# Optimization experiments

Hardware: AMD Instinct MI355X
Metric: run time of the kernel (lower is better)

## Reference

```python
import jax, jax.numpy as jnp
import numpy as np

BATCH, IN_F, OUT_F = 8192, 2048, 2048
LN2 = float(np.log(2.0))


def setup_inputs() -> dict:
    key = jax.random.key(0)
    kx, kw = jax.random.split(key)
    x = jax.random.normal(kx, (BATCH, IN_F), dtype=jnp.float32)
    # kaiming_uniform_(a=sqrt(5)) on (OUT_F, IN_F+1): U(-1/sqrt(fan_in), 1/sqrt(fan_in))
    bound = 1.0 / np.sqrt(IN_F + 1)
    W = jax.random.uniform(kw, (OUT_F, IN_F + 1), dtype=jnp.float32,
                           minval=-bound, maxval=bound)
    W = W.at[:, -1].set(0.0)  # bias column initialized to 0
    return {"x": x, "W": W}


def reference(x, W):
    # UniversalKANNode forward, node_type='add', use_bias=True,
    # function = lshifted_softplus: f(x, w) = w * (softplus(x) - ln2)
    # Append bias ones column: (B, IN_F+1)
    xb = jnp.concatenate([x, jnp.ones((x.shape[0], 1), dtype=x.dtype)], axis=-1)
    phi = jax.nn.softplus(xb) - jnp.asarray(LN2, dtype=x.dtype)  # (B, IN_F+1)
    # sum over input dim of W[o,i] * phi[b,i]  ==  GEMM
    return jnp.einsum("bi,oi->bo", phi, W)  # (B, OUT_F)
```

## Files before the change

### kernel.cpp

```cpp
#include <hip/hip_runtime.h>

#define M_DIM 8192
#define N_DIM 2048
#define K_DIM 2048
#define LN2F 0.69314718055994530942f
#define LOG2EF 1.44269504088896340736f
#define BIAS_PHI 0.62009741f

typedef _Float16 f16x8 __attribute__((ext_vector_type(8)));
typedef float f32x4 __attribute__((ext_vector_type(4)));

__device__ __forceinline__ float softplus_m_ln2(float v) {
    float t = v * LOG2EF;
    float e = __builtin_amdgcn_exp2f(t);
    float r = (__builtin_amdgcn_logf(1.0f + e) - 1.0f) * LN2F;
    return t < 24.0f ? r : v - LN2F;
}

__global__ __launch_bounds__(256) void prep_kernel(const float* __restrict__ x,
                                                   const float* __restrict__ W,
                                                   _Float16* __restrict__ phi,
                                                   _Float16* __restrict__ Wh,
                                                   float* __restrict__ bias) {
    if (blockIdx.x < 8192) {
        size_t i = ((size_t)blockIdx.x * blockDim.x + threadIdx.x) * 8;
        float4 v0 = *(const float4*)(x + i);
        float4 v1 = *(const float4*)(x + i + 4);
        union { _Float16 h[8]; uint4 u; } pk;
        pk.h[0] = (_Float16)softplus_m_ln2(v0.x);
        pk.h[1] = (_Float16)softplus_m_ln2(v0.y);
        pk.h[2] = (_Float16)softplus_m_ln2(v0.z);
        pk.h[3] = (_Float16)softplus_m_ln2(v0.w);
        pk.h[4] = (_Float16)softplus_m_ln2(v1.x);
        pk.h[5] = (_Float16)softplus_m_ln2(v1.y);
        pk.h[6] = (_Float16)softplus_m_ln2(v1.z);
        pk.h[7] = (_Float16)softplus_m_ln2(v1.w);
        *(uint4*)(phi + i) = pk.u;
    } else {
        const int o = blockIdx.x - 8192;
        const float* row = W + (size_t)o * (K_DIM + 1) + threadIdx.x * 8;
        union { _Float16 h[8]; uint4 u; } pk;
#pragma unroll
        for (int j = 0; j < 8; ++j)
            pk.h[j] = (_Float16)row[j];
        *(uint4*)(Wh + (size_t)o * K_DIM + threadIdx.x * 8) = pk.u;
        if (threadIdx.x == 0)
            bias[o] = W[(size_t)o * (K_DIM + 1) + K_DIM] * BIAS_PHI;
    }
}

__global__ __launch_bounds__(256, 2) void kan_gemm(const _Float16* __restrict__ A,
                                                   const _Float16* __restrict__ B,
                                                   const float* __restrict__ bias,
                                                   float* __restrict__ C) {
    __shared__ __align__(16) _Float16 sA[256 * 64];
    __shared__ __align__(16) _Float16 sB[128 * 64];

    const int tid  = threadIdx.x;
    const int lane = tid & 63;
    const int wv   = tid >> 6;

    const size_t Arow0 = (size_t)blockIdx.x * 256;
    const size_t Brow0 = (size_t)blockIdx.y * 128;

    const int r8 = lane >> 3;
    const int lc = (lane & 7) ^ r8;

    const _Float16* gA = A + (Arow0 + wv * 64 + r8) * (size_t)K_DIM + lc * 8;
    _Float16* sAw = &sA[wv * 64 * 64];
    const _Float16* gB = B + (Brow0 + wv * 32 + r8) * (size_t)K_DIM + lc * 8;
    _Float16* sBw = &sB[wv * 32 * 64];

    const int wr = (wv >> 1) * 128;
    const int wc = (wv & 1) * 64;
    const int lr   = lane & 15;
    const int kph0 = ((lane >> 4) ^ (lr & 7)) * 8;

    f32x4 acc[8][4];
#pragma unroll
    for (int i = 0; i < 8; ++i)
#pragma unroll
        for (int j = 0; j < 4; ++j)
            acc[i][j] = (f32x4){0.0f, 0.0f, 0.0f, 0.0f};

    for (int k0 = 0; k0 < K_DIM; k0 += 64) {
        __syncthreads();
#pragma unroll
        for (int j = 0; j < 8; ++j)
            __builtin_amdgcn_global_load_lds(
                (const __attribute__((address_space(1))) void*)(gA + k0 + (size_t)j * 8 * K_DIM),
                (__attribute__((address_space(3))) void*)(sAw + j * 8 * 64), 16, 0, 0);
#pragma unroll
        for (int j = 0; j < 4; ++j)
            __builtin_amdgcn_global_load_lds(
                (const __attribute__((address_space(1))) void*)(gB + k0 + (size_t)j * 8 * K_DIM),
                (__attribute__((address_space(3))) void*)(sBw + j * 8 * 64), 16, 0, 0);
        __syncthreads();

#pragma unroll
        for (int kc = 0; kc < 2; ++kc) {
            const int ko = kph0 ^ (kc * 32);
            f16x8 bfr[4];
#pragma unroll
            for (int ni = 0; ni < 4; ++ni)
                bfr[ni] = *(const f16x8*)&sB[(wc + ni * 16 + lr) * 64 + ko];

#pragma unroll
            for (int mh = 0; mh < 2; ++mh) {
                f16x8 af[4];
#pragma unroll
                for (int mi = 0; mi < 4; ++mi)
                    af[mi] = *(const f16x8*)&sA[(wr + (mh * 4 + mi) * 16 + lr) * 64 + ko];
#pragma unroll
                for (int mi = 0; mi < 4; ++mi)
#pragma unroll
                    for (int ni = 0; ni < 4; ++ni)
                        acc[mh * 4 + mi][ni] = __builtin_amdgcn_mfma_f32_16x16x32_f16(
                            af[mi], bfr[ni], acc[mh * 4 + mi][ni], 0, 0, 0);
            }
        }
    }

    const int crow = (lane >> 4) * 4;
    float bsv[4];
#pragma unroll
    for (int ni = 0; ni < 4; ++ni)
        bsv[ni] = bias[Brow0 + wc + ni * 16 + lr];

#pragma unroll
    for (int mi = 0; mi < 8; ++mi) {
#pragma unroll
        for (int r = 0; r < 4; ++r) {
            float* cp = C + (Arow0 + wr + mi * 16 + crow + r) * (size_t)N_DIM
                        + Brow0 + wc + lr;
#pragma unroll
            for (int ni = 0; ni < 4; ++ni)
                cp[ni * 16] = acc[mi][ni][r] + bsv[ni];
        }
    }
}

extern "C" void kernel_launch(void* const* d_in, const int* in_sizes, int n_in,
                              void* d_out, int out_size, void* d_ws, size_t ws_size,
                              hipStream_t stream) {
    const float* x = (const float*)d_in[0];
    const float* W = (const float*)d_in[1];
    float* out = (float*)d_out;

    char* ws = (char*)d_ws;
    _Float16* phi = (_Float16*)ws;
    _Float16* Wh  = (_Float16*)(ws + (size_t)M_DIM * K_DIM * sizeof(_Float16));
    float* bias   = (float*)(ws + (size_t)M_DIM * K_DIM * sizeof(_Float16)
                                + (size_t)N_DIM * K_DIM * sizeof(_Float16));

    prep_kernel<<<8192 + 2048, 256, 0, stream>>>(x, W, phi, Wh, bias);
    dim3 grid(M_DIM / 256, N_DIM / 128);
    kan_gemm<<<grid, 256, 0, stream>>>(phi, Wh, bias, out);
}
```

Measured before the change: 185.6 us.

## Double-buffer GEMM LDS tiles with 8-wave 256x256 blocks and interleaved prefetch

The GEMM moves from 4 waves on a 256x128 tile to 8 waves on a 256x256 tile. The LDS A and B tiles are double-buffered, and the next K-slice's global-to-LDS loads are spread across four MFMA phases separated by barriers and raised s_setprio. The aim is to hide global load latency behind MFMA work, which the old single-buffer loop exposed with two barriers per iteration, and to improve data reuse per block. In exchange, LDS use grows to 128KB per block, which likely allows only one block per CU despite launch_bounds(512,2). Each iteration also now has more barriers.

```diff
diff --git a/kernel.cpp b/kernel.cpp
--- a/kernel.cpp
+++ b/kernel.cpp
@@ -49,30 +49,31 @@
     }
 }
 
-__global__ __launch_bounds__(256, 2) void kan_gemm(const _Float16* __restrict__ A,
+#define GLL(gp, lp)                                                                     \
+    __builtin_amdgcn_global_load_lds((const __attribute__((address_space(1))) void*)(gp), \
+                                     (__attribute__((address_space(3))) void*)(lp), 16, 0, 0)
+
+__global__ __launch_bounds__(512, 2) void kan_gemm(const _Float16* __restrict__ A,
                                                    const _Float16* __restrict__ B,
                                                    const float* __restrict__ bias,
                                                    float* __restrict__ C) {
-    __shared__ __align__(16) _Float16 sA[256 * 64];
-    __shared__ __align__(16) _Float16 sB[128 * 64];
+    __shared__ __align__(16) _Float16 sA[2][256 * 64];
+    __shared__ __align__(16) _Float16 sB[2][256 * 64];
 
     const int tid  = threadIdx.x;
     const int lane = tid & 63;
     const int wv   = tid >> 6;
+    const int wm   = wv >> 2;
+    const int wn   = wv & 3;
 
     const size_t Arow0 = (size_t)blockIdx.x * 256;
-    const size_t Brow0 = (size_t)blockIdx.y * 128;
+    const size_t Bcol0 = (size_t)blockIdx.y * 256;
 
     const int r8 = lane >> 3;
     const int lc = (lane & 7) ^ r8;
-
-    const _Float16* gA = A + (Arow0 + wv * 64 + r8) * (size_t)K_DIM + lc * 8;
-    _Float16* sAw = &sA[wv * 64 * 64];
-    const _Float16* gB = B + (Brow0 + wv * 32 + r8) * (size_t)K_DIM + lc * 8;
-    _Float16* sBw = &sB[wv * 32 * 64];
-
-    const int wr = (wv >> 1) * 128;
-    const int wc = (wv & 1) * 64;
+    const _Float16* gA = A + (Arow0 + wv * 32 + r8) * (size_t)K_DIM + lc * 8;
+    const _Float16* gB = B + (Bcol0 + wv * 32 + r8) * (size_t)K_DIM + lc * 8;
+
     const int lr   = lane & 15;
     const int kph0 = ((lane >> 4) ^ (lr & 7)) * 8;
 
@@ -83,56 +84,139 @@
         for (int j = 0; j < 4; ++j)
             acc[i][j] = (f32x4){0.0f, 0.0f, 0.0f, 0.0f};
 
-    for (int k0 = 0; k0 < K_DIM; k0 += 64) {
-        __syncthreads();
-#pragma unroll
-        for (int j = 0; j < 8; ++j)
-            __builtin_amdgcn_global_load_lds(
-                (const __attribute__((address_space(1))) void*)(gA + k0 + (size_t)j * 8 * K_DIM),
-                (__attribute__((address_space(3))) void*)(sAw + j * 8 * 64), 16, 0, 0);
-#pragma unroll
-        for (int j = 0; j < 4; ++j)
-            __builtin_amdgcn_global_load_lds(
-                (const __attribute__((address_space(1))) void*)(gB + k0 + (size_t)j * 8 * K_DIM),
-                (__attribute__((address_space(3))) void*)(sBw + j * 8 * 64), 16, 0, 0);
-        __syncthreads();
-
-#pragma unroll
-        for (int kc = 0; kc < 2; ++kc) {
-            const int ko = kph0 ^ (kc * 32);
-            f16x8 bfr[4];
-#pragma unroll
-            for (int ni = 0; ni < 4; ++ni)
-                bfr[ni] = *(const f16x8*)&sB[(wc + ni * 16 + lr) * 64 + ko];
-
-#pragma unroll
-            for (int mh = 0; mh < 2; ++mh) {
-                f16x8 af[4];
-#pragma unroll
-                for (int mi = 0; mi < 4; ++mi)
-                    af[mi] = *(const f16x8*)&sA[(wr + (mh * 4 + mi) * 16 + lr) * 64 + ko];
-#pragma unroll
-                for (int mi = 0; mi < 4; ++mi)
-#pragma unroll
-                    for (int ni = 0; ni < 4; ++ni)
-                        acc[mh * 4 + mi][ni] = __builtin_amdgcn_mfma_f32_16x16x32_f16(
-                            af[mi], bfr[ni], acc[mh * 4 + mi][ni], 0, 0, 0);
-            }
-        }
+#pragma unroll
+    for (int j = 0; j < 4; ++j)
+        GLL(gA + (size_t)j * 8 * K_DIM, &sA[0][(wv * 32 + j * 8) * 64]);
+#pragma unroll
+    for (int j = 0; j < 4; ++j)
+        GLL(gB + (size_t)j * 8 * K_DIM, &sB[0][(wv * 32 + j * 8) * 64]);
+    asm volatile("s_waitcnt vmcnt(0)" ::: "memory");
+    __builtin_amdgcn_s_barrier();
+
+    f16x8 afr[4][2];
+    f16x8 bfr[2][2];
+
+    for (int t = 0; t < 32; ++t) {
+        const int d = t & 1;
+        const _Float16* sAd = sA[d];
+        const _Float16* sBd = sB[d];
+        _Float16* dA = sA[d ^ 1];
+        _Float16* dB = sB[d ^ 1];
+        const size_t kn = (size_t)(t + 1) * 64;
+        const bool more = (t + 1) < 32;
+
+#pragma unroll
+        for (int mi = 0; mi < 4; ++mi)
+#pragma unroll
+            for (int kc = 0; kc < 2; ++kc)
+                afr[mi][kc] = *(const f16x8*)&sAd[(wm * 128 + mi * 16 + lr) * 64 + (kph0 ^ (kc * 32))];
+#pragma unroll
+        for (int ni = 0; ni < 2; ++ni)
+#pragma unroll
+            for (int kc = 0; kc < 2; ++kc)
+                bfr[ni][kc] = *(const f16x8*)&sBd[(wn * 64 + ni * 16 + lr) * 64 + (kph0 ^ (kc * 32))];
+        if (more) {
+            GLL(gA + kn + (size_t)0 * 8 * K_DIM, &dA[(wv * 32 + 0) * 64]);
+            GLL(gA + kn + (size_t)1 * 8 * K_DIM, &dA[(wv * 32 + 8) * 64]);
+        }
+        __builtin_amdgcn_s_barrier();
+        asm volatile("s_waitcnt lgkmcnt(0)" ::: "memory");
+        __builtin_amdgcn_s_setprio(1);
+#pragma unroll
+        for (int kc = 0; kc < 2; ++kc)
+#pragma unroll
+            for (int mi = 0; mi < 4; ++mi)
+#pragma unroll
+                for (int ni = 0; ni < 2; ++ni)
+                    acc[mi][ni] = __builtin_amdgcn_mfma_f32_16x16x32_f16(
+                        afr[mi][kc], bfr[ni][kc], acc[mi][ni], 0, 0, 0);
+        __builtin_amdgcn_s_setprio(0);
+        __builtin_amdgcn_s_barrier();
+
+#pragma unroll
+        for (int ni = 0; ni < 2; ++ni)
+#pragma unroll
+            for (int kc = 0; kc < 2; ++kc)
+                bfr[ni][kc] = *(const f16x8*)&sBd[(wn * 64 + 32 + ni * 16 + lr) * 64 + (kph0 ^ (kc * 32))];
+        if (more) {
+            GLL(gA + kn + (size_t)2 * 8 * K_DIM, &dA[(wv * 32 + 16) * 64]);
+            GLL(gA + kn + (size_t)3 * 8 * K_DIM, &dA[(wv * 32 + 24) * 64]);
+        }
+        __builtin_amdgcn_s_barrier();
+        asm volatile("s_waitcnt lgkmcnt(0)" ::: "memory");
+        __builtin_amdgcn_s_setprio(1);
+#pragma unroll
+        for (int kc = 0; kc < 2; ++kc)
+#pragma unroll
+            for (int mi = 0; mi < 4; ++mi)
+#pragma unroll
+                for (int ni = 0; ni < 2; ++ni)
+                    acc[mi][2 + ni] = __builtin_amdgcn_mfma_f32_16x16x32_f16(
+                        afr[mi][kc], bfr[ni][kc], acc[mi][2 + ni], 0, 0, 0);
+        __builtin_amdgcn_s_setprio(0);
+        __builtin_amdgcn_s_barrier();
+
+#pragma unroll
+        for (int mi = 0; mi < 4; ++mi)
+#pragma unroll
+            for (int kc = 0; kc < 2; ++kc)
+                afr[mi][kc] = *(const f16x8*)&sAd[(wm * 128 + 64 + mi * 16 + lr) * 64 + (kph0 ^ (kc * 32))];
+        if (more) {
+            GLL(gB + kn + (size_t)0 * 8 * K_DIM, &dB[(wv * 32 + 0) * 64]);
+            GLL(gB + kn + (size_t)1 * 8 * K_DIM, &dB[(wv * 32 + 8) * 64]);
+        }
+        __builtin_amdgcn_s_barrier();
+        asm volatile("s_waitcnt lgkmcnt(0)" ::: "memory");
+        __builtin_amdgcn_s_setprio(1);
+#pragma unroll
+        for (int kc = 0; kc < 2; ++kc)
+#pragma unroll
+            for (int mi = 0; mi < 4; ++mi)
+#pragma unroll
+                for (int ni = 0; ni < 2; ++ni)
+                    acc[4 + mi][2 + ni] = __builtin_amdgcn_mfma_f32_16x16x32_f16(
+                        afr[mi][kc], bfr[ni][kc], acc[4 + mi][2 + ni], 0, 0, 0);
+        __builtin_amdgcn_s_setprio(0);
+        __builtin_amdgcn_s_barrier();
+
+#pragma unroll
+        for (int ni = 0; ni < 2; ++ni)
+#pragma unroll
+            for (int kc = 0; kc < 2; ++kc)
+                bfr[ni][kc] = *(const f16x8*)&sBd[(wn * 64 + ni * 16 + lr) * 64 + (kph0 ^ (kc * 32))];
+        if (more) {
+            GLL(gB + kn + (size_t)2 * 8 * K_DIM, &dB[(wv * 32 + 16) * 64]);
+            GLL(gB + kn + (size_t)3 * 8 * K_DIM, &dB[(wv * 32 + 24) * 64]);
+        }
+        __builtin_amdgcn_s_barrier();
+        asm volatile("s_waitcnt lgkmcnt(0)" ::: "memory");
+        __builtin_amdgcn_s_setprio(1);
+#pragma unroll
+        for (int kc = 0; kc < 2; ++kc)
+#pragma unroll
+            for (int mi = 0; mi < 4; ++mi)
+#pragma unroll
+                for (int ni = 0; ni < 2; ++ni)
+                    acc[4 + mi][ni] = __builtin_amdgcn_mfma_f32_16x16x32_f16(
+                        afr[mi][kc], bfr[ni][kc], acc[4 + mi][ni], 0, 0, 0);
+        __builtin_amdgcn_s_setprio(0);
+
+        asm volatile("s_waitcnt vmcnt(0)" ::: "memory");
+        __builtin_amdgcn_s_barrier();
     }
 
     const int crow = (lane >> 4) * 4;
     float bsv[4];
 #pragma unroll
     for (int ni = 0; ni < 4; ++ni)
-        bsv[ni] = bias[Brow0 + wc + ni * 16 + lr];
+        bsv[ni] = bias[Bcol0 + wn * 64 + ni * 16 + lr];
 
 #pragma unroll
     for (int mi = 0; mi < 8; ++mi) {
 #pragma unroll
         for (int r = 0; r < 4; ++r) {
-            float* cp = C + (Arow0 + wr + mi * 16 + crow + r) * (size_t)N_DIM
-                        + Brow0 + wc + lr;
+            float* cp = C + (Arow0 + wm * 128 + mi * 16 + crow + r) * (size_t)N_DIM
+                        + Bcol0 + wn * 64 + lr;
 #pragma unroll
             for (int ni = 0; ni < 4; ++ni)
                 cp[ni * 16] = acc[mi][ni][r] + bsv[ni];
@@ -154,6 +238,6 @@
                                 + (size_t)N_DIM * K_DIM * sizeof(_Float16));
 
     prep_kernel<<<8192 + 2048, 256, 0, stream>>>(x, W, phi, Wh, bias);
-    dim3 grid(M_DIM / 256, N_DIM / 128);
-    kan_gemm<<<grid, 256, 0, stream>>>(phi, Wh, bias, out);
-}
+    dim3 grid(M_DIM / 256, N_DIM / 256);
+    kan_gemm<<<grid, 512, 0, stream>>>(phi, Wh, bias, out);
+}
```

Result: no change. 188.1 us (+1.3%).

## Rewrite GEMM as 256x256 tile, 8-wave, double-buffered LDS pipeline with interleaved loads

Applied to the files above, without the earlier changes.

The GEMM tile grows from 256x128 to 256x256 with 512 threads (8 waves in a 2x4 layout). LDS is double-buffered, and global-to-LDS loads are interleaved with MFMA quadrants using explicit vmcnt/lgkmcnt waits, barriers and setprio, in a ping-pong style schedule. The aim is to hide global load latency behind MFMA work and to raise arithmetic intensity per tile. In exchange, LDS use grows to 128KB per block and the hand-tuned wait counts are fragile; an error in them would produce wrong results.

```diff
diff --git a/kernel.cpp b/kernel.cpp
--- a/kernel.cpp
+++ b/kernel.cpp
@@ -49,30 +49,80 @@
     }
 }
 
-__global__ __launch_bounds__(256, 2) void kan_gemm(const _Float16* __restrict__ A,
+#define GLL(gp, lp)                                                                     \
+    __builtin_amdgcn_global_load_lds((const __attribute__((address_space(1))) void*)(gp), \
+                                     (__attribute__((address_space(3))) void*)(lp), 16, 0, 0)
+
+#define BAR   __builtin_amdgcn_s_barrier()
+#define LGKM0 asm volatile("s_waitcnt lgkmcnt(0)" ::: "memory")
+#define VM(n) asm volatile("s_waitcnt vmcnt(" #n ")" ::: "memory")
+#define PRIO1 __builtin_amdgcn_s_setprio(1)
+#define PRIO0 __builtin_amdgcn_s_setprio(0)
+
+#define READ_A(dst, d, roff)                                                             \
+    _Pragma("unroll") for (int kc = 0; kc < 2; ++kc)                                     \
+    _Pragma("unroll") for (int mi = 0; mi < 4; ++mi)                                     \
+        dst[mi][kc] = *(const f16x8*)&sA[d][(wm * 128 + (roff) + mi * 16 + lr) * 64 + (kph0 ^ (kc * 32))];
+
+#define READ_B(dst, d, coff)                                                             \
+    _Pragma("unroll") for (int kc = 0; kc < 2; ++kc)                                     \
+    _Pragma("unroll") for (int ni = 0; ni < 2; ++ni)                                     \
+        dst[ni][kc] = *(const f16x8*)&sB[d][(wn * 64 + (coff) + ni * 16 + lr) * 64 + (kph0 ^ (kc * 32))];
+
+#define MFMA_Q(AF, BF, AI, BJ)                                                           \
+    _Pragma("unroll") for (int kc = 0; kc < 2; ++kc)                                     \
+    _Pragma("unroll") for (int mi = 0; mi < 4; ++mi)                                     \
+    _Pragma("unroll") for (int ni = 0; ni < 2; ++ni)                                     \
+        acc[(AI) + mi][(BJ) + ni] = __builtin_amdgcn_mfma_f32_16x16x32_f16(              \
+            AF[mi][kc], BF[ni][kc], acc[(AI) + mi][(BJ) + ni], 0, 0, 0);
+
+#define GLL_A(half, buf, kt)                                                             \
+    do {                                                                                 \
+        GLL(gAj[2 * (half)] + (size_t)(kt) * 64, &sA[buf][rA[2 * (half)] * 64]);         \
+        GLL(gAj[2 * (half) + 1] + (size_t)(kt) * 64, &sA[buf][rA[2 * (half) + 1] * 64]); \
+    } while (0)
+#define GLL_B(half, buf, kt)                                                             \
+    do {                                                                                 \
+        GLL(gBj[2 * (half)] + (size_t)(kt) * 64, &sB[buf][rB[2 * (half)] * 64]);         \
+        GLL(gBj[2 * (half) + 1] + (size_t)(kt) * 64, &sB[buf][rB[2 * (half) + 1] * 64]); \
+    } while (0)
+
+__global__ __launch_bounds__(512, 2) void kan_gemm(const _Float16* __restrict__ A,
                                                    const _Float16* __restrict__ B,
                                                    const float* __restrict__ bias,
                                                    float* __restrict__ C) {
-    __shared__ __align__(16) _Float16 sA[256 * 64];
-    __shared__ __align__(16) _Float16 sB[128 * 64];
+    __shared__ __align__(16) _Float16 sA[2][256 * 64];
+    __shared__ __align__(16) _Float16 sB[2][256 * 64];
 
     const int tid  = threadIdx.x;
     const int lane = tid & 63;
     const int wv   = tid >> 6;
+    const int wm   = wv >> 2;
+    const int wn   = wv & 3;
 
     const size_t Arow0 = (size_t)blockIdx.x * 256;
-    const size_t Brow0 = (size_t)blockIdx.y * 128;
+    const size_t Bcol0 = (size_t)blockIdx.y * 256;
 
     const int r8 = lane >> 3;
     const int lc = (lane & 7) ^ r8;
 
-    const _Float16* gA = A + (Arow0 + wv * 64 + r8) * (size_t)K_DIM + lc * 8;
-    _Float16* sAw = &sA[wv * 64 * 64];
-    const _Float16* gB = B + (Brow0 + wv * 32 + r8) * (size_t)K_DIM + lc * 8;
-    _Float16* sBw = &sB[wv * 32 * 64];
-
-    const int wr = (wv >> 1) * 128;
-    const int wc = (wv & 1) * 64;
+    const int g0 = wv * 2, g1 = wv * 2 + 1;
+    const int rA[4] = {(g0 >> 3) * 128 + (g0 & 7) * 8,
+                       (g1 >> 3) * 128 + (g1 & 7) * 8,
+                       (g0 >> 3) * 128 + (g0 & 7) * 8 + 64,
+                       (g1 >> 3) * 128 + (g1 & 7) * 8 + 64};
+    const int rB[4] = {(g0 >> 2) * 64 + (g0 & 3) * 8,
+                       (g1 >> 2) * 64 + (g1 & 3) * 8,
+                       (g0 >> 2) * 64 + (g0 & 3) * 8 + 32,
+                       (g1 >> 2) * 64 + (g1 & 3) * 8 + 32};
+    const _Float16* gAj[4];
+    const _Float16* gBj[4];
+#pragma unroll
+    for (int j = 0; j < 4; ++j) {
+        gAj[j] = A + (Arow0 + rA[j] + r8) * (size_t)K_DIM + lc * 8;
+        gBj[j] = B + (Bcol0 + rB[j] + r8) * (size_t)K_DIM + lc * 8;
+    }
+
     const int lr   = lane & 15;
     const int kph0 = ((lane >> 4) ^ (lr & 7)) * 8;
 
@@ -83,59 +133,80 @@
         for (int j = 0; j < 4; ++j)
             acc[i][j] = (f32x4){0.0f, 0.0f, 0.0f, 0.0f};
 
-    for (int k0 = 0; k0 < K_DIM; k0 += 64) {
-        __syncthreads();
-#pragma unroll
-        for (int j = 0; j < 8; ++j)
-            __builtin_amdgcn_global_load_lds(
-                (const __attribute__((address_space(1))) void*)(gA + k0 + (size_t)j * 8 * K_DIM),
-                (__attribute__((address_space(3))) void*)(sAw + j * 8 * 64), 16, 0, 0);
-#pragma unroll
-        for (int j = 0; j < 4; ++j)
-            __builtin_amdgcn_global_load_lds(
-                (const __attribute__((address_space(1))) void*)(gB + k0 + (size_t)j * 8 * K_DIM),
-                (__attribute__((address_space(3))) void*)(sBw + j * 8 * 64), 16, 0, 0);
-        __syncthreads();
-
-#pragma unroll
-        for (int kc = 0; kc < 2; ++kc) {
-            const int ko = kph0 ^ (kc * 32);
-            f16x8 bfr[4];
-#pragma unroll
-            for (int ni = 0; ni < 4; ++ni)
-                bfr[ni] = *(const f16x8*)&sB[(wc + ni * 16 + lr) * 64 + ko];
-
-#pragma unroll
-            for (int mh = 0; mh < 2; ++mh) {
-                f16x8 af[4];
-#pragma unroll
-                for (int mi = 0; mi < 4; ++mi)
-                    af[mi] = *(const f16x8*)&sA[(wr + (mh * 4 + mi) * 16 + lr) * 64 + ko];
-#pragma unroll
-                for (int mi = 0; mi < 4; ++mi)
-#pragma unroll
-                    for (int ni = 0; ni < 4; ++ni)
-                        acc[mh * 4 + mi][ni] = __builtin_amdgcn_mfma_f32_16x16x32_f16(
-                            af[mi], bfr[ni], acc[mh * 4 + mi][ni], 0, 0, 0);
-            }
-        }
+    f16x8 afr0[4][2], afr1[4][2];
+    f16x8 bfr0[2][2], bfr1[2][2];
+
+    GLL_A(0, 0, 0); GLL_B(0, 0, 0); GLL_A(1, 0, 0); GLL_B(1, 0, 0);
+    GLL_A(0, 1, 1); GLL_B(0, 1, 1); GLL_A(1, 1, 1);
+    VM(10); BAR;
+
+    for (int i = 0; i < 15; ++i) {
+        const int t1 = 2 * i + 1;
+        const int n0 = 2 * i + 2, n1 = 2 * i + 3;
+        READ_A(afr0, 0, 0); READ_B(bfr0, 0, 0);
+        GLL_B(1, 1, t1);
+        BAR; LGKM0; PRIO1; MFMA_Q(afr0, bfr0, 0, 0); PRIO0; VM(10); BAR;
+        READ_A(afr1, 0, 64);
+        GLL_A(0, 0, n0);
+        BAR; LGKM0; PRIO1; MFMA_Q(afr1, bfr0, 4, 0); PRIO0; VM(10); BAR;
+        READ_B(bfr1, 0, 32);
+        GLL_B(0, 0, n0);
+        BAR; LGKM0; PRIO1; MFMA_Q(afr1, bfr1, 4, 2); PRIO0; BAR;
+        GLL_A(1, 0, n0);
+        BAR; PRIO1; MFMA_Q(afr0, bfr1, 0, 2); PRIO0; VM(10); BAR;
+        READ_A(afr0, 1, 0); READ_B(bfr0, 1, 0);
+        GLL_B(1, 0, n0);
+        BAR; LGKM0; PRIO1; MFMA_Q(afr0, bfr0, 0, 0); PRIO0; VM(10); BAR;
+        READ_A(afr1, 1, 64);
+        GLL_A(0, 1, n1);
+        BAR; LGKM0; PRIO1; MFMA_Q(afr1, bfr0, 4, 0); PRIO0; VM(10); BAR;
+        READ_B(bfr1, 1, 32);
+        GLL_B(0, 1, n1);
+        BAR; LGKM0; PRIO1; MFMA_Q(afr1, bfr1, 4, 2); PRIO0; BAR;
+        GLL_A(1, 1, n1);
+        BAR; PRIO1; MFMA_Q(afr0, bfr1, 0, 2); PRIO0; VM(10); BAR;
+    }
+
+    {
+        READ_A(afr0, 0, 0); READ_B(bfr0, 0, 0);
+        GLL_B(1, 1, 31);
+        BAR; LGKM0; PRIO1; MFMA_Q(afr0, bfr0, 0, 0); PRIO0; VM(10); BAR;
+
+        READ_A(afr1, 0, 64);
+        BAR; LGKM0; PRIO1; MFMA_Q(afr1, bfr0, 4, 0); PRIO0; VM(8); BAR;
+
+        READ_B(bfr1, 0, 32);
+        BAR; LGKM0; PRIO1; MFMA_Q(afr1, bfr1, 4, 2); PRIO0; BAR;
+
+        BAR; PRIO1; MFMA_Q(afr0, bfr1, 0, 2); PRIO0; VM(4); BAR;
+
+        READ_A(afr0, 1, 0); READ_B(bfr0, 1, 0);
+        BAR; LGKM0; PRIO1; MFMA_Q(afr0, bfr0, 0, 0); PRIO0; VM(2); BAR;
+
+        READ_A(afr1, 1, 64);
+        BAR; LGKM0; PRIO1; MFMA_Q(afr1, bfr0, 4, 0); PRIO0; VM(0); BAR;
+
+        READ_B(bfr1, 1, 32);
+        BAR; LGKM0; PRIO1; MFMA_Q(afr1, bfr1, 4, 2); PRIO0; BAR;
+
+        BAR; PRIO1; MFMA_Q(afr0, bfr1, 0, 2); PRIO0;
     }
 
     const int crow = (lane >> 4) * 4;
     float bsv[4];
 #pragma unroll
-    for (int ni = 0; ni < 4; ++ni)
-        bsv[ni] = bias[Brow0 + wc + ni * 16 + lr];
-
-#pragma unroll
-    for (int mi = 0; mi < 8; ++mi) {
+    for (int bj = 0; bj < 4; ++bj)
+        bsv[bj] = bias[Bcol0 + wn * 64 + (bj >> 1) * 32 + (bj & 1) * 16 + lr];
+
+#pragma unroll
+    for (int ai = 0; ai < 8; ++ai) {
 #pragma unroll
         for (int r = 0; r < 4; ++r) {
-            float* cp = C + (Arow0 + wr + mi * 16 + crow + r) * (size_t)N_DIM
-                        + Brow0 + wc + lr;
-#pragma unroll
-            for (int ni = 0; ni < 4; ++ni)
-                cp[ni * 16] = acc[mi][ni][r] + bsv[ni];
+            float* cp = C + (Arow0 + wm * 128 + (ai >> 2) * 64 + (ai & 3) * 16 + crow + r) * (size_t)N_DIM
+                        + Bcol0 + wn * 64 + lr;
+#pragma unroll
+            for (int bj = 0; bj < 4; ++bj)
+                cp[(bj >> 1) * 32 + (bj & 1) * 16] = acc[ai][bj][r] + bsv[bj];
         }
     }
 }
@@ -154,6 +225,6 @@
                                 + (size_t)N_DIM * K_DIM * sizeof(_Float16));
 
     prep_kernel<<<8192 + 2048, 256, 0, stream>>>(x, W, phi, Wh, bias);
-    dim3 grid(M_DIM / 256, N_DIM / 128);
-    kan_gemm<<<grid, 256, 0, stream>>>(phi, Wh, bias, out);
-}
+    dim3 grid(M_DIM / 256, N_DIM / 256);
+    kan_gemm<<<grid, 512, 0, stream>>>(phi, Wh, bias, out);
+}
```

Result: no change. 186.6 us (+0.5%).
